# Optimization experiments

Measured on AMD Instinct MI355X. Metric: run time of the kernel, lower is better.

Reference implementation:

```python
import jax, jax.numpy as jnp
import numpy as np

B, S, D = 8, 2048, 512  # batch, seq_len, lstm_hidden_dim


def setup_inputs() -> dict:
    key = jax.random.key(0)
    kq, kk, kv = jax.random.split(key, 3)
    return {
        "query": jax.random.normal(kq, (B, S, D), dtype=jnp.float32),
        "key": jax.random.normal(kk, (B, S, D), dtype=jnp.float32),
        "value": jax.random.normal(kv, (B, S, D), dtype=jnp.float32),
    }


def reference(query, key, value):
    hidden_dim = query.shape[-1]
    scale = 1.0 / jnp.sqrt(jnp.asarray(hidden_dim, dtype=jnp.float32))
    # scores: [B, S, S]
    scores = jnp.einsum("bqd,bkd->bqk", query, key) * scale
    attention_weights = jax.nn.softmax(scores, axis=-1)
    context = jnp.einsum("bqk,bkd->bqd", attention_weights, value)
    return (context, attention_weights)
```

## Files before the change

### kernel.cpp

```cpp
#include <hip/hip_runtime.h>


constexpr int BATCH = 8;
constexpr int SEQ = 2048;
constexpr int DIM = 512;

typedef __attribute__((ext_vector_type(8))) short bh8;
typedef __attribute__((ext_vector_type(4))) float f4acc;

__device__ __forceinline__ short f2bf(float f) {
  union { float f; unsigned u; } v;
  v.f = f;
  unsigned r = (v.u + 0x7FFFu + ((v.u >> 16) & 1u)) >> 16;
  return (short)r;
}

__global__ __launch_bounds__(256) void transpose_v_kernel(
    const float* __restrict__ V, unsigned short* __restrict__ Vt) {
  __shared__ float tile[32][33];
  const int s0 = blockIdx.x * 32, d0 = blockIdx.y * 32, b = blockIdx.z;
  const float* Vb = V + (size_t)b * SEQ * DIM;
  unsigned short* Vtb = Vt + (size_t)b * DIM * SEQ;
  const int tx = threadIdx.x & 31, ty = threadIdx.x >> 5;
  for (int r = 0; r < 32; r += 8)
    tile[ty + r][tx] = Vb[(size_t)(s0 + ty + r) * DIM + (d0 + tx)];
  __syncthreads();
  for (int r = 0; r < 32; r += 8)
    Vtb[(size_t)(d0 + ty + r) * SEQ + (s0 + tx)] =
        (unsigned short)f2bf(tile[tx][ty + r]);
}

__global__ __launch_bounds__(256) void scores_kernel(
    const float* __restrict__ Q, const float* __restrict__ K,
    float* __restrict__ W) {
  __shared__ short As[128][40];
  __shared__ short Bs[128][40];
  const int bm = blockIdx.x, bn = blockIdx.y, b = blockIdx.z;
  const int tid = threadIdx.x, lane = tid & 63, wave = tid >> 6;
  const int wm = (wave & 1) * 64, wn = (wave >> 1) * 64;
  const float* Qb = Q + (size_t)b * SEQ * DIM + (size_t)(bm * 128) * DIM;
  const float* Kb = K + (size_t)b * SEQ * DIM + (size_t)(bn * 128) * DIM;
  f4acc acc[4][4] = {};
  const int fr = lane & 15, fk = (lane >> 4) * 8;
  for (int k0 = 0; k0 < DIM; k0 += 32) {
    for (int it = 0; it < 4; ++it) {
      int idx = it * 256 + tid;
      int row = idx >> 3, c4 = (idx & 7) * 4;
      float4 q = *(const float4*)(Qb + (size_t)row * DIM + k0 + c4);
      float4 k = *(const float4*)(Kb + (size_t)row * DIM + k0 + c4);
      short* ap = &As[row][c4];
      ap[0] = f2bf(q.x); ap[1] = f2bf(q.y); ap[2] = f2bf(q.z); ap[3] = f2bf(q.w);
      short* bp = &Bs[row][c4];
      bp[0] = f2bf(k.x); bp[1] = f2bf(k.y); bp[2] = f2bf(k.z); bp[3] = f2bf(k.w);
    }
    __syncthreads();
    bh8 af[4], bfrag[4];
    for (int i = 0; i < 4; ++i) af[i]    = *(const bh8*)&As[wm + i * 16 + fr][fk];
    for (int i = 0; i < 4; ++i) bfrag[i] = *(const bh8*)&Bs[wn + i * 16 + fr][fk];
    for (int mi = 0; mi < 4; ++mi)
      for (int ni = 0; ni < 4; ++ni)
        acc[mi][ni] = __builtin_amdgcn_mfma_f32_16x16x32_bf16(
            af[mi], bfrag[ni], acc[mi][ni], 0, 0, 0);
    __syncthreads();
  }
  const float scale = 0.044194173824159216f;
  float* Wb = W + (size_t)b * SEQ * SEQ + (size_t)(bm * 128) * SEQ + bn * 128;
  const int cc = lane & 15, rr = (lane >> 4) * 4;
  for (int mi = 0; mi < 4; ++mi)
    for (int ni = 0; ni < 4; ++ni)
      for (int r = 0; r < 4; ++r) {
        int row = wm + mi * 16 + rr + r;
        int col = wn + ni * 16 + cc;
        Wb[(size_t)row * SEQ + col] = acc[mi][ni][r] * scale;
      }
}

__global__ __launch_bounds__(256) void softmax_kernel(float* __restrict__ W) {
  float* Wr = W + (size_t)blockIdx.x * SEQ;
  const int tid = threadIdx.x, lane = tid & 63, wave = tid >> 6;
  float4 a = ((const float4*)Wr)[tid];
  float4 c = ((const float4*)Wr)[tid + 256];
  float m = fmaxf(fmaxf(fmaxf(a.x, a.y), fmaxf(a.z, a.w)),
                  fmaxf(fmaxf(c.x, c.y), fmaxf(c.z, c.w)));
  for (int off = 32; off > 0; off >>= 1) m = fmaxf(m, __shfl_xor(m, off));
  __shared__ float redm[4];
  if (lane == 0) redm[wave] = m;
  __syncthreads();
  m = fmaxf(fmaxf(redm[0], redm[1]), fmaxf(redm[2], redm[3]));
  a.x = __expf(a.x - m); a.y = __expf(a.y - m);
  a.z = __expf(a.z - m); a.w = __expf(a.w - m);
  c.x = __expf(c.x - m); c.y = __expf(c.y - m);
  c.z = __expf(c.z - m); c.w = __expf(c.w - m);
  float s = (a.x + a.y + a.z + a.w) + (c.x + c.y + c.z + c.w);
  for (int off = 32; off > 0; off >>= 1) s += __shfl_xor(s, off);
  __shared__ float reds[4];
  if (lane == 0) reds[wave] = s;
  __syncthreads();
  s = reds[0] + reds[1] + reds[2] + reds[3];
  const float inv = 1.0f / s;
  a.x *= inv; a.y *= inv; a.z *= inv; a.w *= inv;
  c.x *= inv; c.y *= inv; c.z *= inv; c.w *= inv;
  ((float4*)Wr)[tid] = a;
  ((float4*)Wr)[tid + 256] = c;
}

__global__ __launch_bounds__(256) void context_kernel(
    const float* __restrict__ W, const unsigned short* __restrict__ Vt,
    float* __restrict__ C) {
  __shared__ short As[128][40];
  __shared__ short Bs[128][40];
  const int bm = blockIdx.x, bn = blockIdx.y, b = blockIdx.z;
  const int tid = threadIdx.x, lane = tid & 63, wave = tid >> 6;
  const int wm = (wave & 1) * 64, wn = (wave >> 1) * 64;
  const float* Ab = W + (size_t)b * SEQ * SEQ + (size_t)(bm * 128) * SEQ;
  const unsigned short* Vtb =
      Vt + (size_t)b * DIM * SEQ + (size_t)(bn * 128) * SEQ;
  f4acc acc[4][4] = {};
  const int fr = lane & 15, fk = (lane >> 4) * 8;
  for (int k0 = 0; k0 < SEQ; k0 += 32) {
    for (int it = 0; it < 4; ++it) {
      int idx = it * 256 + tid;
      int row = idx >> 3, c4 = (idx & 7) * 4;
      float4 w4 = *(const float4*)(Ab + (size_t)row * SEQ + k0 + c4);
      short* ap = &As[row][c4];
      ap[0] = f2bf(w4.x); ap[1] = f2bf(w4.y); ap[2] = f2bf(w4.z); ap[3] = f2bf(w4.w);
    }
    for (int it = 0; it < 2; ++it) {
      int idx = it * 256 + tid;
      int row = idx >> 2, c8 = (idx & 3) * 8;
      bh8 v = *(const bh8*)(Vtb + (size_t)row * SEQ + k0 + c8);
      *(bh8*)&Bs[row][c8] = v;
    }
    __syncthreads();
    bh8 af[4], bfrag[4];
    for (int i = 0; i < 4; ++i) af[i]    = *(const bh8*)&As[wm + i * 16 + fr][fk];
    for (int i = 0; i < 4; ++i) bfrag[i] = *(const bh8*)&Bs[wn + i * 16 + fr][fk];
    for (int mi = 0; mi < 4; ++mi)
      for (int ni = 0; ni < 4; ++ni)
        acc[mi][ni] = __builtin_amdgcn_mfma_f32_16x16x32_bf16(
            af[mi], bfrag[ni], acc[mi][ni], 0, 0, 0);
    __syncthreads();
  }
  float* Cb = C + (size_t)b * SEQ * DIM + (size_t)(bm * 128) * DIM + bn * 128;
  const int cc = lane & 15, rr = (lane >> 4) * 4;
  for (int mi = 0; mi < 4; ++mi)
    for (int ni = 0; ni < 4; ++ni)
      for (int r = 0; r < 4; ++r) {
        int row = wm + mi * 16 + rr + r;
        int col = wn + ni * 16 + cc;
        Cb[(size_t)row * DIM + col] = acc[mi][ni][r];
      }
}

extern "C" void kernel_launch(void* const* d_in, const int* in_sizes, int n_in,
                              void* d_out, int out_size, void* d_ws,
                              size_t ws_size, hipStream_t stream) {
  const float* Q = (const float*)d_in[0];
  const float* K = (const float*)d_in[1];
  const float* V = (const float*)d_in[2];
  float* C = (float*)d_out;
  float* W = (float*)d_out + (size_t)BATCH * SEQ * DIM;
  unsigned short* Vt = (unsigned short*)d_ws;

  transpose_v_kernel<<<dim3(SEQ / 32, DIM / 32, BATCH), 256, 0, stream>>>(V, Vt);
  scores_kernel<<<dim3(SEQ / 128, SEQ / 128, BATCH), 256, 0, stream>>>(Q, K, W);
  softmax_kernel<<<dim3(BATCH * SEQ), 256, 0, stream>>>(W);
  context_kernel<<<dim3(SEQ / 128, DIM / 128, BATCH), 256, 0, stream>>>(W, Vt, C);
}
```

Before: 401.3 us.

## Pre-convert operands to bf16 and stage GEMM tiles via direct global-to-LDS loads

Adds a kernel that converts Q (with the softmax scale folded in) and K to bf16 up front, and makes softmax also emit a bf16 copy of the weights. Both GEMMs then share one templated body that loads bf16 tiles straight into LDS with global_load_lds instead of loading fp32 and converting in registers. This halves operand read traffic, removes repeated per-tile conversion in the scores GEMM, and drops ALU work from the inner loops. The cost is an extra conversion pass, extra workspace, and an extra bf16 write of the full weight matrix. The unpadded LDS layout may also cause bank conflicts.

```diff
diff --git a/kernel.cpp b/kernel.cpp
--- a/kernel.cpp
+++ b/kernel.cpp
@@ -4,6 +4,7 @@
 constexpr int BATCH = 8;
 constexpr int SEQ = 2048;
 constexpr int DIM = 512;
+constexpr size_t QK_ELEMS = (size_t)BATCH * SEQ * DIM;
 
 typedef __attribute__((ext_vector_type(8))) short bh8;
 typedef __attribute__((ext_vector_type(4))) float f4acc;
@@ -13,6 +14,30 @@
   v.f = f;
   unsigned r = (v.u + 0x7FFFu + ((v.u >> 16) & 1u)) >> 16;
   return (short)r;
+}
+
+__device__ __forceinline__ void glds16(const unsigned short* g,
+                                       unsigned short* l) {
+  __builtin_amdgcn_global_load_lds(
+      (const __attribute__((address_space(1))) unsigned int*)g,
+      (__attribute__((address_space(3))) unsigned int*)l, 16, 0, 0);
+}
+
+__global__ __launch_bounds__(256) void convert_qk_kernel(
+    const float* __restrict__ Q, const float* __restrict__ K,
+    unsigned short* __restrict__ Qbf, unsigned short* __restrict__ Kbf) {
+  const size_t i = ((size_t)blockIdx.x * 256 + threadIdx.x) * 8;
+  const float sc = blockIdx.y ? 1.0f : 0.044194173824159216f;
+  const float* src = blockIdx.y ? K : Q;
+  unsigned short* dst = blockIdx.y ? Kbf : Qbf;
+  float4 a = *(const float4*)(src + i);
+  float4 b = *(const float4*)(src + i + 4);
+  bh8 o;
+  o[0] = f2bf(a.x * sc); o[1] = f2bf(a.y * sc);
+  o[2] = f2bf(a.z * sc); o[3] = f2bf(a.w * sc);
+  o[4] = f2bf(b.x * sc); o[5] = f2bf(b.y * sc);
+  o[6] = f2bf(b.z * sc); o[7] = f2bf(b.w * sc);
+  *(bh8*)(dst + i) = o;
 }
 
 __global__ __launch_bounds__(256) void transpose_v_kernel(
@@ -30,53 +55,73 @@
         (unsigned short)f2bf(tile[tx][ty + r]);
 }
 
-__global__ __launch_bounds__(256) void scores_kernel(
-    const float* __restrict__ Q, const float* __restrict__ K,
-    float* __restrict__ W) {
-  __shared__ short As[128][40];
-  __shared__ short Bs[128][40];
-  const int bm = blockIdx.x, bn = blockIdx.y, b = blockIdx.z;
+template <int KDIM, int NSTRIDE>
+__device__ __forceinline__ void gemm_nt_body(
+    const unsigned short* __restrict__ Arows,
+    const unsigned short* __restrict__ Brows,
+    float* __restrict__ Cout,
+    unsigned short* As, unsigned short* Bs) {
   const int tid = threadIdx.x, lane = tid & 63, wave = tid >> 6;
   const int wm = (wave & 1) * 64, wn = (wave >> 1) * 64;
-  const float* Qb = Q + (size_t)b * SEQ * DIM + (size_t)(bm * 128) * DIM;
-  const float* Kb = K + (size_t)b * SEQ * DIM + (size_t)(bn * 128) * DIM;
+  const int srow = wave * 32 + (lane >> 2);
+  const int scol = (lane & 3) * 8;
+  const unsigned short* Ag = Arows + (size_t)srow * KDIM + scol;
+  const unsigned short* Bg = Brows + (size_t)srow * KDIM + scol;
+  unsigned short* Al = As + srow * 32 + scol;
+  unsigned short* Bl = Bs + srow * 32 + scol;
   f4acc acc[4][4] = {};
   const int fr = lane & 15, fk = (lane >> 4) * 8;
-  for (int k0 = 0; k0 < DIM; k0 += 32) {
-    for (int it = 0; it < 4; ++it) {
-      int idx = it * 256 + tid;
-      int row = idx >> 3, c4 = (idx & 7) * 4;
-      float4 q = *(const float4*)(Qb + (size_t)row * DIM + k0 + c4);
-      float4 k = *(const float4*)(Kb + (size_t)row * DIM + k0 + c4);
-      short* ap = &As[row][c4];
-      ap[0] = f2bf(q.x); ap[1] = f2bf(q.y); ap[2] = f2bf(q.z); ap[3] = f2bf(q.w);
-      short* bp = &Bs[row][c4];
-      bp[0] = f2bf(k.x); bp[1] = f2bf(k.y); bp[2] = f2bf(k.z); bp[3] = f2bf(k.w);
-    }
+  for (int k0 = 0; k0 < KDIM; k0 += 32) {
+    glds16(Ag + k0, Al);
+    glds16(Ag + k0 + (size_t)16 * KDIM, Al + 16 * 32);
+    glds16(Bg + k0, Bl);
+    glds16(Bg + k0 + (size_t)16 * KDIM, Bl + 16 * 32);
     __syncthreads();
-    bh8 af[4], bfrag[4];
-    for (int i = 0; i < 4; ++i) af[i]    = *(const bh8*)&As[wm + i * 16 + fr][fk];
-    for (int i = 0; i < 4; ++i) bfrag[i] = *(const bh8*)&Bs[wn + i * 16 + fr][fk];
+    bh8 af[4], bf[4];
+    for (int i = 0; i < 4; ++i) af[i] = *(const bh8*)(As + (wm + i * 16 + fr) * 32 + fk);
+    for (int i = 0; i < 4; ++i) bf[i] = *(const bh8*)(Bs + (wn + i * 16 + fr) * 32 + fk);
     for (int mi = 0; mi < 4; ++mi)
       for (int ni = 0; ni < 4; ++ni)
         acc[mi][ni] = __builtin_amdgcn_mfma_f32_16x16x32_bf16(
-            af[mi], bfrag[ni], acc[mi][ni], 0, 0, 0);
+            af[mi], bf[ni], acc[mi][ni], 0, 0, 0);
     __syncthreads();
   }
-  const float scale = 0.044194173824159216f;
-  float* Wb = W + (size_t)b * SEQ * SEQ + (size_t)(bm * 128) * SEQ + bn * 128;
   const int cc = lane & 15, rr = (lane >> 4) * 4;
   for (int mi = 0; mi < 4; ++mi)
     for (int ni = 0; ni < 4; ++ni)
-      for (int r = 0; r < 4; ++r) {
-        int row = wm + mi * 16 + rr + r;
-        int col = wn + ni * 16 + cc;
-        Wb[(size_t)row * SEQ + col] = acc[mi][ni][r] * scale;
-      }
+      for (int r = 0; r < 4; ++r)
+        Cout[(size_t)(wm + mi * 16 + rr + r) * NSTRIDE + (wn + ni * 16 + cc)] =
+            acc[mi][ni][r];
 }
 
-__global__ __launch_bounds__(256) void softmax_kernel(float* __restrict__ W) {
+__global__ __launch_bounds__(256) void scores_kernel(
+    const unsigned short* __restrict__ Qbf, const unsigned short* __restrict__ Kbf,
+    float* __restrict__ W) {
+  __shared__ unsigned short As[128 * 32];
+  __shared__ unsigned short Bs[128 * 32];
+  const int bm = blockIdx.x, bn = blockIdx.y, b = blockIdx.z;
+  gemm_nt_body<DIM, SEQ>(
+      Qbf + ((size_t)b * SEQ + bm * 128) * DIM,
+      Kbf + ((size_t)b * SEQ + bn * 128) * DIM,
+      W + (size_t)b * SEQ * SEQ + (size_t)(bm * 128) * SEQ + bn * 128, As, Bs);
+}
+
+__global__ __launch_bounds__(256) void context_kernel(
+    const unsigned short* __restrict__ Wbf, const unsigned short* __restrict__ Vt,
+    float* __restrict__ C) {
+  __shared__ unsigned short As[128 * 32];
+  __shared__ unsigned short Bs[128 * 32];
+  const int bm = blockIdx.x, bn = blockIdx.y, b = blockIdx.z;
+  gemm_nt_body<SEQ, DIM>(
+      Wbf + ((size_t)b * SEQ + bm * 128) * SEQ,
+      Vt + ((size_t)b * DIM + bn * 128) * SEQ,
+      C + (size_t)b * SEQ * DIM + (size_t)(bm * 128) * DIM + bn * 128, As, Bs);
+}
+
+__global__ __launch_bounds__(256) void softmax_kernel(
+    float* __restrict__ W, unsigned short* __restrict__ Wbf) {
   float* Wr = W + (size_t)blockIdx.x * SEQ;
+  unsigned short* Wbr = Wbf + (size_t)blockIdx.x * SEQ;
   const int tid = threadIdx.x, lane = tid & 63, wave = tid >> 6;
   float4 a = ((const float4*)Wr)[tid];
   float4 c = ((const float4*)Wr)[tid + 256];
@@ -102,54 +147,10 @@
   c.x *= inv; c.y *= inv; c.z *= inv; c.w *= inv;
   ((float4*)Wr)[tid] = a;
   ((float4*)Wr)[tid + 256] = c;
-}
-
-__global__ __launch_bounds__(256) void context_kernel(
-    const float* __restrict__ W, const unsigned short* __restrict__ Vt,
-    float* __restrict__ C) {
-  __shared__ short As[128][40];
-  __shared__ short Bs[128][40];
-  const int bm = blockIdx.x, bn = blockIdx.y, b = blockIdx.z;
-  const int tid = threadIdx.x, lane = tid & 63, wave = tid >> 6;
-  const int wm = (wave & 1) * 64, wn = (wave >> 1) * 64;
-  const float* Ab = W + (size_t)b * SEQ * SEQ + (size_t)(bm * 128) * SEQ;
-  const unsigned short* Vtb =
-      Vt + (size_t)b * DIM * SEQ + (size_t)(bn * 128) * SEQ;
-  f4acc acc[4][4] = {};
-  const int fr = lane & 15, fk = (lane >> 4) * 8;
-  for (int k0 = 0; k0 < SEQ; k0 += 32) {
-    for (int it = 0; it < 4; ++it) {
-      int idx = it * 256 + tid;
-      int row = idx >> 3, c4 = (idx & 7) * 4;
-      float4 w4 = *(const float4*)(Ab + (size_t)row * SEQ + k0 + c4);
-      short* ap = &As[row][c4];
-      ap[0] = f2bf(w4.x); ap[1] = f2bf(w4.y); ap[2] = f2bf(w4.z); ap[3] = f2bf(w4.w);
-    }
-    for (int it = 0; it < 2; ++it) {
-      int idx = it * 256 + tid;
-      int row = idx >> 2, c8 = (idx & 3) * 8;
-      bh8 v = *(const bh8*)(Vtb + (size_t)row * SEQ + k0 + c8);
-      *(bh8*)&Bs[row][c8] = v;
-    }
-    __syncthreads();
-    bh8 af[4], bfrag[4];
-    for (int i = 0; i < 4; ++i) af[i]    = *(const bh8*)&As[wm + i * 16 + fr][fk];
-    for (int i = 0; i < 4; ++i) bfrag[i] = *(const bh8*)&Bs[wn + i * 16 + fr][fk];
-    for (int mi = 0; mi < 4; ++mi)
-      for (int ni = 0; ni < 4; ++ni)
-        acc[mi][ni] = __builtin_amdgcn_mfma_f32_16x16x32_bf16(
-            af[mi], bfrag[ni], acc[mi][ni], 0, 0, 0);
-    __syncthreads();
-  }
-  float* Cb = C + (size_t)b * SEQ * DIM + (size_t)(bm * 128) * DIM + bn * 128;
-  const int cc = lane & 15, rr = (lane >> 4) * 4;
-  for (int mi = 0; mi < 4; ++mi)
-    for (int ni = 0; ni < 4; ++ni)
-      for (int r = 0; r < 4; ++r) {
-        int row = wm + mi * 16 + rr + r;
-        int col = wn + ni * 16 + cc;
-        Cb[(size_t)row * DIM + col] = acc[mi][ni][r];
-      }
+  short4 ba = {f2bf(a.x), f2bf(a.y), f2bf(a.z), f2bf(a.w)};
+  short4 bc = {f2bf(c.x), f2bf(c.y), f2bf(c.z), f2bf(c.w)};
+  ((short4*)Wbr)[tid] = ba;
+  ((short4*)Wbr)[tid + 256] = bc;
 }
 
 extern "C" void kernel_launch(void* const* d_in, const int* in_sizes, int n_in,
@@ -159,11 +160,16 @@
   const float* K = (const float*)d_in[1];
   const float* V = (const float*)d_in[2];
   float* C = (float*)d_out;
-  float* W = (float*)d_out + (size_t)BATCH * SEQ * DIM;
-  unsigned short* Vt = (unsigned short*)d_ws;
+  float* W = (float*)d_out + QK_ELEMS;
+  unsigned short* Qbf = (unsigned short*)d_ws;
+  unsigned short* Kbf = Qbf + QK_ELEMS;
+  unsigned short* Vt  = Kbf + QK_ELEMS;
+  unsigned short* Wbf = Vt + QK_ELEMS;
 
+  convert_qk_kernel<<<dim3((unsigned)(QK_ELEMS / 8 / 256), 2), 256, 0, stream>>>(
+      Q, K, Qbf, Kbf);
   transpose_v_kernel<<<dim3(SEQ / 32, DIM / 32, BATCH), 256, 0, stream>>>(V, Vt);
-  scores_kernel<<<dim3(SEQ / 128, SEQ / 128, BATCH), 256, 0, stream>>>(Q, K, W);
-  softmax_kernel<<<dim3(BATCH * SEQ), 256, 0, stream>>>(W);
-  context_kernel<<<dim3(SEQ / 128, DIM / 128, BATCH), 256, 0, stream>>>(W, Vt, C);
+  scores_kernel<<<dim3(SEQ / 128, SEQ / 128, BATCH), 256, 0, stream>>>(Qbf, Kbf, W);
+  softmax_kernel<<<dim3(BATCH * SEQ), 256, 0, stream>>>(W, Wbf);
+  context_kernel<<<dim3(SEQ / 128, DIM / 128, BATCH), 256, 0, stream>>>(Wbf, Vt, C);
 }
```

After: 385.6 us. 1.04x faster.
